# Kernel tuning notes

Measured on AMD Instinct MI355X. Metric: run time of the kernel, lower is better.

## Reference

```python
import jax, jax.numpy as jnp
import numpy as np

H = 128            # hidden_channels
HM = 2 * H         # _inner_mlp_mult * H
N = 50000          # num nodes
E = 400000         # num edges
M = 800000         # num node-edge incidences (2 per edge)
BN_EPS = 1e-5


def _bn_relu(x, g, b):
    # BatchNorm1d in training mode: population stats over the batch dim, then affine + ReLU
    m = x.mean(0)
    v = ((x - m) ** 2).mean(0)
    return jax.nn.relu((x - m) * jax.lax.rsqrt(v + BN_EPS) * g + b)


def setup_inputs() -> dict:
    key = jax.random.key(0)
    ks = jax.random.split(key, 12)
    node_rep = jax.random.normal(ks[0], (N, H), dtype=jnp.float32)
    edge_rep = jax.random.normal(ks[1], (E, H), dtype=jnp.float32)
    src = jax.random.randint(ks[2], (M,), 0, N, dtype=jnp.int32)
    dst = jax.random.randint(ks[3], (M,), 0, E, dtype=jnp.int32)
    node2edge_index = jnp.stack([src, dst], 0)

    def lin(k, fan_in, fan_out):
        return jax.random.normal(k, (fan_in, fan_out), dtype=jnp.float32) / np.sqrt(fan_in)

    return {
        "node_rep": node_rep,
        "edge_rep": edge_rep,
        "node2edge_index": node2edge_index,
        # lvl_mlp_1: Linear(2H->H, no bias), BN(H), ReLU
        "Wa": lin(ks[4], 2 * H, H), "ga": jnp.ones((H,)), "ba": jnp.zeros((H,)),
        # lvl_mlp_2: Linear(H->2H), BN, ReLU, Linear(2H->H), BN, ReLU
        "Wb1": lin(ks[5], H, HM), "gb1": jnp.ones((HM,)), "bb1": jnp.zeros((HM,)),
        "Wb2": lin(ks[6], HM, H), "gb2": jnp.ones((H,)), "bb2": jnp.zeros((H,)),
        # lift_mlp: Linear(H->2H), BN, ReLU, Linear(2H->H), BN, ReLU
        "Wl1": lin(ks[7], H, HM), "gl1": jnp.ones((HM,)), "bl1": jnp.zeros((HM,)),
        "Wl2": lin(ks[8], HM, H), "gl2": jnp.ones((H,)), "bl2": jnp.zeros((H,)),
        "eps1": jnp.zeros(()), "eps2": jnp.zeros(()),
    }


def reference(node_rep, edge_rep, node2edge_index,
              Wa, ga, ba,
              Wb1, gb1, bb1, Wb2, gb2, bb2,
              Wl1, gl1, bl1, Wl2, gl2, bl2,
              eps1, eps2):
    src = node2edge_index[0]  # node index per incidence
    dst = node2edge_index[1]  # edge index per incidence

    # node -> edge gather + scatter_sum
    node2edge_val = node_rep[src]                                   # [M, H]
    lift_aggr = jax.ops.segment_sum(node2edge_val, dst, num_segments=E)  # [E, H]

    # lvl_mlp_1 on concatenated edge features
    lvl_aggr_edge = _bn_relu(jnp.concatenate([lift_aggr, edge_rep], -1) @ Wa, ga, ba)  # [E, H]

    # edge -> node gather + scatter_sum
    lvl_aggr = jax.ops.segment_sum(lvl_aggr_edge[dst], src, num_segments=N)  # [N, H]

    # lvl_mlp_2
    hn = (1.0 + eps1) * node_rep + lvl_aggr
    node_out = _bn_relu(_bn_relu(hn @ Wb1, gb1, bb1) @ Wb2, gb2, bb2)

    # lift_mlp
    he = (1.0 + eps2) * edge_rep + lift_aggr
    edge_out = _bn_relu(_bn_relu(he @ Wl1, gl1, bl1) @ Wl2, gl2, bl2)

    return node_out, edge_out
```

## Files before the change

kernel.cpp:

```cpp
#include <hip/hip_runtime.h>
#include <cstdint>
#include <cstddef>


typedef __bf16 bf16_t;
typedef __bf16 bf16x4 __attribute__((ext_vector_type(4)));
typedef __bf16 bf16x8 __attribute__((ext_vector_type(8)));
typedef float f32x4 __attribute__((ext_vector_type(4)));

__device__ __forceinline__ void atomAddF(float* p, float v) {
  unsafeAtomicAdd(p, v);
}

__device__ __forceinline__ void gload16(const void* g, void* l) {
  __builtin_amdgcn_global_load_lds(
      (const __attribute__((address_space(1))) unsigned int*)g,
      (__attribute__((address_space(3))) unsigned int*)l, 16, 0, 0);
}


__global__ __launch_bounds__(256) void k_hist(
    const int* __restrict__ src, const int* __restrict__ dst, int M,
    int* __restrict__ cnt_e, int* __restrict__ cnt_n) {
  int i = blockIdx.x * blockDim.x + threadIdx.x;
  if (i >= M) return;
  atomicAdd(cnt_e + dst[i], 1);
  atomicAdd(cnt_n + src[i], 1);
}

__global__ __launch_bounds__(256) void k_scan_block(
    const int* __restrict__ in, int* __restrict__ out, int* __restrict__ bsum,
    int L) {
  __shared__ int sh[256];
  int t = threadIdx.x;
  int base = (blockIdx.x * 256 + t) * 4;
  int v[4];
#pragma unroll
  for (int j = 0; j < 4; ++j) v[j] = (base + j < L) ? in[base + j] : 0;
  int tsum = v[0] + v[1] + v[2] + v[3];
  sh[t] = tsum;
  __syncthreads();
#pragma unroll
  for (int off = 1; off < 256; off <<= 1) {
    int x = (t >= off) ? sh[t - off] : 0;
    __syncthreads();
    sh[t] += x;
    __syncthreads();
  }
  int excl = sh[t] - tsum;
  if (t == 255) bsum[blockIdx.x] = sh[255];
  int run = excl;
#pragma unroll
  for (int j = 0; j < 4; ++j) {
    if (base + j < L) out[base + j] = run;
    run += v[j];
  }
}

__global__ __launch_bounds__(1024) void k_scan_top(int* __restrict__ bsum,
                                                   int nb) {
  __shared__ int sh[1024];
  __shared__ int running;
  int t = threadIdx.x;
  if (t == 0) running = 0;
  __syncthreads();
  for (int c = 0; c < nb; c += 1024) {
    int i = c + t;
    int v = (i < nb) ? bsum[i] : 0;
    sh[t] = v;
    __syncthreads();
#pragma unroll
    for (int off = 1; off < 1024; off <<= 1) {
      int x = (t >= off) ? sh[t - off] : 0;
      __syncthreads();
      sh[t] += x;
      __syncthreads();
    }
    int r = running;
    if (i < nb) bsum[i] = r + sh[t] - v;
    __syncthreads();
    if (t == 1023) running = r + sh[1023];
    __syncthreads();
  }
}

__global__ __launch_bounds__(256) void k_scan_add(int* __restrict__ out,
                                                  const int* __restrict__ bsum,
                                                  int L) {
  int base = (blockIdx.x * 256 + threadIdx.x) * 4;
  int add = bsum[blockIdx.x];
#pragma unroll
  for (int j = 0; j < 4; ++j)
    if (base + j < L) out[base + j] += add;
}

__global__ void k_settail(int* off_e, int E, int* off_n, int N, int M) {
  off_e[E] = M;
  off_n[N] = M;
}

__global__ __launch_bounds__(256) void k_fill(
    const int* __restrict__ src, const int* __restrict__ dst, int M,
    const int* __restrict__ off_e, int* __restrict__ fill_e,
    int* __restrict__ csr_e, const int* __restrict__ off_n,
    int* __restrict__ fill_n, int* __restrict__ csr_n) {
  int i = blockIdx.x * blockDim.x + threadIdx.x;
  if (i >= M) return;
  int s = src[i], d = dst[i];
  int pe = off_e[d] + atomicAdd(fill_e + d, 1);
  csr_e[pe] = s;
  int pn = off_n[s] + atomicAdd(fill_n + s, 1);
  csr_n[pn] = d;
}

__global__ __launch_bounds__(256) void k_wconv(const float* __restrict__ W,
                                               bf16_t* __restrict__ Wt, int K,
                                               int NC) {
  int idx = blockIdx.x * blockDim.x + threadIdx.x;
  if (idx >= K * NC) return;
  int k = idx / NC, n = idx % NC;
  Wt[(size_t)n * K + k] = (bf16_t)W[idx];
}

__global__ __launch_bounds__(256) void k_gather1(
    const float* __restrict__ node, const int* __restrict__ off_e,
    const int* __restrict__ csr_e, bf16_t* __restrict__ lift, int E) {
  int e = blockIdx.x * 8 + (threadIdx.x >> 5);
  if (e >= E) return;
  int l = threadIdx.x & 31;
  int b = off_e[e], en = off_e[e + 1];
  float4 acc = make_float4(0.f, 0.f, 0.f, 0.f);
  for (int j = b; j < en; ++j) {
    int r = csr_e[j];
    float4 v = *(const float4*)(node + (size_t)r * 128 + l * 4);
    acc.x += v.x; acc.y += v.y; acc.z += v.z; acc.w += v.w;
  }
  bf16x4 o;
  o[0] = (bf16_t)acc.x; o[1] = (bf16_t)acc.y;
  o[2] = (bf16_t)acc.z; o[3] = (bf16_t)acc.w;
  *(bf16x4*)(lift + (size_t)e * 128 + l * 4) = o;
}

__global__ __launch_bounds__(256) void k_gather2(
    const bf16_t* __restrict__ Y1, const float* __restrict__ st,
    const float* __restrict__ node, const int* __restrict__ off_n,
    const int* __restrict__ csr_n, const float* __restrict__ eps1p,
    bf16_t* __restrict__ hn, int N) {
  int n = blockIdx.x * 16 + (threadIdx.x >> 4);
  if (n >= N) return;
  int l = threadIdx.x & 15;
  float a1 = 1.0f + eps1p[0];
  float4 s0 = *(const float4*)(st + l * 8);
  float4 s1 = *(const float4*)(st + l * 8 + 4);
  float4 t0 = *(const float4*)(st + 128 + l * 8);
  float4 t1 = *(const float4*)(st + 128 + l * 8 + 4);
  float acc[8] = {0.f, 0.f, 0.f, 0.f, 0.f, 0.f, 0.f, 0.f};
  int b = off_n[n], en = off_n[n + 1];
  for (int j = b; j < en; ++j) {
    int r = csr_n[j];
    bf16x8 y = *(const bf16x8*)(Y1 + (size_t)r * 128 + l * 8);
    acc[0] += fmaxf(fmaf((float)y[0], s0.x, t0.x), 0.f);
    acc[1] += fmaxf(fmaf((float)y[1], s0.y, t0.y), 0.f);
    acc[2] += fmaxf(fmaf((float)y[2], s0.z, t0.z), 0.f);
    acc[3] += fmaxf(fmaf((float)y[3], s0.w, t0.w), 0.f);
    acc[4] += fmaxf(fmaf((float)y[4], s1.x, t1.x), 0.f);
    acc[5] += fmaxf(fmaf((float)y[5], s1.y, t1.y), 0.f);
    acc[6] += fmaxf(fmaf((float)y[6], s1.z, t1.z), 0.f);
    acc[7] += fmaxf(fmaf((float)y[7], s1.w, t1.w), 0.f);
  }
  float4 n0 = *(const float4*)(node + (size_t)n * 128 + l * 8);
  float4 n1 = *(const float4*)(node + (size_t)n * 128 + l * 8 + 4);
  bf16x8 hb;
  hb[0] = (bf16_t)fmaf(a1, n0.x, acc[0]);
  hb[1] = (bf16_t)fmaf(a1, n0.y, acc[1]);
  hb[2] = (bf16_t)fmaf(a1, n0.z, acc[2]);
  hb[3] = (bf16_t)fmaf(a1, n0.w, acc[3]);
  hb[4] = (bf16_t)fmaf(a1, n1.x, acc[4]);
  hb[5] = (bf16_t)fmaf(a1, n1.y, acc[5]);
  hb[6] = (bf16_t)fmaf(a1, n1.z, acc[6]);
  hb[7] = (bf16_t)fmaf(a1, n1.w, acc[7]);
  *(bf16x8*)(hn + (size_t)n * 128 + l * 8) = hb;
}


__global__ void k_bnfin(const float* __restrict__ sums, int C, int R,
                        const float* __restrict__ g, const float* __restrict__ b,
                        float* __restrict__ st) {
  int c = blockIdx.x * blockDim.x + threadIdx.x;
  if (c >= C) return;
  float invR = 1.f / (float)R;
  float mean = sums[c] * invR;
  float var = fmaxf(sums[C + c] * invR - mean * mean, 0.f);
  float s = g[c] * rsqrtf(var + 1e-5f);
  st[c] = s;
  st[C + c] = fmaf(-mean, s, b[c]);
}

__global__ __launch_bounds__(256) void k_bnrelu_out(
    const bf16_t* __restrict__ Y, const float* __restrict__ st, long R,
    float* __restrict__ out) {
  long t = (long)blockIdx.x * blockDim.x + threadIdx.x;
  long idx = t * 8;
  if (idx >= R * 128) return;
  int c = (int)(idx & 127);
  bf16x8 y = *(const bf16x8*)(Y + idx);
  float4 s0 = *(const float4*)(st + c);
  float4 s1 = *(const float4*)(st + c + 4);
  float4 t0 = *(const float4*)(st + 128 + c);
  float4 t1 = *(const float4*)(st + 128 + c + 4);
  float4 o0, o1;
  o0.x = fmaxf(fmaf((float)y[0], s0.x, t0.x), 0.f);
  o0.y = fmaxf(fmaf((float)y[1], s0.y, t0.y), 0.f);
  o0.z = fmaxf(fmaf((float)y[2], s0.z, t0.z), 0.f);
  o0.w = fmaxf(fmaf((float)y[3], s0.w, t0.w), 0.f);
  o1.x = fmaxf(fmaf((float)y[4], s1.x, t1.x), 0.f);
  o1.y = fmaxf(fmaf((float)y[5], s1.y, t1.y), 0.f);
  o1.z = fmaxf(fmaf((float)y[6], s1.z, t1.z), 0.f);
  o1.w = fmaxf(fmaf((float)y[7], s1.w, t1.w), 0.f);
  *(float4*)(out + idx) = o0;
  *(float4*)(out + idx + 4) = o1;
}

template <int K, int NC, int TRANSFORM>
__global__ __launch_bounds__(256, 2) void k_gemm_rb(
    const bf16_t* __restrict__ A, const bf16_t* __restrict__ Wt,
    const float* __restrict__ st, float* __restrict__ gstats,
    bf16_t* __restrict__ Y, int R) {
  constexpr int K2 = K * 2;
  constexpr int KF = K / 32;
  constexpr int CTW = NC / 64;
  constexpr int STG = K2 / 64;
  constexpr int TILEB = 64 * K2;
  __shared__ __align__(16) char ldsc[65536];
  const int tid = threadIdx.x;

  for (int p = tid * 16; p < 65536; p += 4096)
    *(float4*)(ldsc + p) = *(const float4*)((const char*)Wt + p);
  __syncthreads();
  const int wv = tid >> 6, lane = tid & 63, quad = lane >> 4, l16 = lane & 15;
  bf16x8 breg[CTW][KF];
#pragma unroll
  for (int ct = 0; ct < CTW; ++ct) {
    const int col = wv * (NC / 4) + ct * 16 + l16;
#pragma unroll
    for (int f = 0; f < KF; ++f)
      breg[ct][f] = *(const bf16x8*)(ldsc + col * K2 + f * 64 + quad * 16);
  }
  __syncthreads();

  int stg_off[STG], stg_row[STG];
#pragma unroll
  for (int j = 0; j < STG; ++j) {
    const int p = j * 1024 + lane * 16;
    const int rl = p / K2;
    const int cg = ((p & (K2 - 1)) >> 4) ^ (rl & 7);
    stg_row[j] = rl;
    stg_off[j] = rl * K2 + cg * 16;
  }
  const int ntiles = (R + 63) >> 6;
  auto stage = [&](int t, int b) {
    char* db = ldsc + b * TILEB + wv * (16 * K2);
    if (t * 64 + 64 <= R) {
      const char* srcb = (const char*)A + (size_t)(t * 64 + wv * 16) * K2;
#pragma unroll
      for (int j = 0; j < STG; ++j) gload16(srcb + stg_off[j], db + j * 1024);
    } else {
#pragma unroll
      for (int j = 0; j < STG; ++j) {
        int g = t * 64 + wv * 16 + stg_row[j];
        if (g > R - 1) g = R - 1;
        gload16((const char*)A + (size_t)g * K2 +
                    (stg_off[j] - stg_row[j] * K2),
                db + j * 1024);
      }
    }
  };

  float csum[CTW], csq[CTW];
#pragma unroll
  for (int ct = 0; ct < CTW; ++ct) { csum[ct] = 0.f; csq[ct] = 0.f; }

  int t = blockIdx.x, b = 0;
  if (t < ntiles) stage(t, 0);
  __syncthreads();
  for (; t < ntiles; t += gridDim.x) {
    const int tn = t + gridDim.x;
    if (tn < ntiles) stage(tn, b ^ 1);
    const char* Ab = ldsc + b * TILEB;
    f32x4 acc[4][CTW] = {};
#pragma unroll
    for (int f = 0; f < KF; ++f) {
      const int csw = ((f * 4 + quad) ^ (l16 & 7)) * 16;
      float4 s0, s1, u0, u1;
      if constexpr (TRANSFORM != 0) {
        const int k = f * 32 + quad * 8;
        s0 = *(const float4*)(st + k);
        s1 = *(const float4*)(st + k + 4);
        u0 = *(const float4*)(st + K + k);
        u1 = *(const float4*)(st + K + k + 4);
      }
#pragma unroll
      for (int rg = 0; rg < 4; ++rg) {
        bf16x8 a = *(const bf16x8*)(Ab + (rg * 16 + l16) * K2 + csw);
        if constexpr (TRANSFORM != 0) {
          bf16x8 o;
          o[0] = (bf16_t)fmaxf(fmaf((float)a[0], s0.x, u0.x), 0.f);
          o[1] = (bf16_t)fmaxf(fmaf((float)a[1], s0.y, u0.y), 0.f);
          o[2] = (bf16_t)fmaxf(fmaf((float)a[2], s0.z, u0.z), 0.f);
          o[3] = (bf16_t)fmaxf(fmaf((float)a[3], s0.w, u0.w), 0.f);
          o[4] = (bf16_t)fmaxf(fmaf((float)a[4], s1.x, u1.x), 0.f);
          o[5] = (bf16_t)fmaxf(fmaf((float)a[5], s1.y, u1.y), 0.f);
          o[6] = (bf16_t)fmaxf(fmaf((float)a[6], s1.z, u1.z), 0.f);
          o[7] = (bf16_t)fmaxf(fmaf((float)a[7], s1.w, u1.w), 0.f);
          a = o;
        }
#pragma unroll
        for (int ct = 0; ct < CTW; ++ct)
          acc[rg][ct] = __builtin_amdgcn_mfma_f32_16x16x32_bf16(
              a, breg[ct][f], acc[rg][ct], 0, 0, 0);
      }
    }
#pragma unroll
    for (int rg = 0; rg < 4; ++rg) {
      const int rowb = t * 64 + rg * 16 + quad * 4;
#pragma unroll
      for (int ct = 0; ct < CTW; ++ct) {
        const int col = wv * (NC / 4) + ct * 16 + l16;
#pragma unroll
        for (int r = 0; r < 4; ++r) {
          const int row = rowb + r;
          if (row < R) {
            const float v = acc[rg][ct][r];
            Y[(size_t)row * NC + col] = (bf16_t)v;
            csum[ct] += v;
            csq[ct] += v * v;
          }
        }
      }
    }
    __syncthreads();
    b ^= 1;
  }
#pragma unroll
  for (int ct = 0; ct < CTW; ++ct) {
    float s = csum[ct], q = csq[ct];
    s += __shfl_xor(s, 16, 64);
    s += __shfl_xor(s, 32, 64);
    q += __shfl_xor(q, 16, 64);
    q += __shfl_xor(q, 32, 64);
    if (quad == 0) {
      const int col = wv * (NC / 4) + ct * 16 + l16;
      atomAddF(gstats + col, s);
      atomAddF(gstats + NC + col, q);
    }
  }
}

__global__ __launch_bounds__(256, 2) void k_gemm_cat_rb(
    const bf16_t* __restrict__ lift, const float* __restrict__ edge,
    const bf16_t* __restrict__ Wt, const float* __restrict__ eps2p,
    float* __restrict__ gstats, bf16_t* __restrict__ Y,
    bf16_t* __restrict__ he, int R) {
  constexpr int KF = 8, CTW = 2;
  __shared__ __align__(16) char ldsc[65536];
  const int tid = threadIdx.x;
  for (int p = tid * 16; p < 65536; p += 4096)
    *(float4*)(ldsc + p) = *(const float4*)((const char*)Wt + p);
  __syncthreads();
  const int wv = tid >> 6, lane = tid & 63, quad = lane >> 4, l16 = lane & 15;
  bf16x8 breg[CTW][KF];
#pragma unroll
  for (int ct = 0; ct < CTW; ++ct) {
    const int col = wv * 32 + ct * 16 + l16;
#pragma unroll
    for (int f = 0; f < KF; ++f)
      breg[ct][f] = *(const bf16x8*)(ldsc + col * 512 + f * 64 + quad * 16);
  }
  __syncthreads();

  const float a2 = 1.0f + eps2p[0];
  const int hi = lane >> 5;
  const int c32 = lane & 31;
  const int ntiles = (R + 63) >> 6;
  float4 ereg[8];
  bf16x4 lreg[8];
  auto loadRegs = [&](int t) {
#pragma unroll
    for (int it = 0; it < 8; ++it) {
      int g = t * 64 + wv * 16 + it * 2 + hi;
      if (g > R - 1) g = R - 1;
      ereg[it] = *(const float4*)(edge + (size_t)g * 128 + c32 * 4);
      lreg[it] = *(const bf16x4*)(lift + (size_t)g * 128 + c32 * 4);
    }
  };
  auto stageHe = [&](int t, int b) {
    char* db = ldsc + b * 32768;
#pragma unroll
    for (int it = 0; it < 8; ++it) {
      const int rl = wv * 16 + it * 2 + hi;
      const int g = t * 64 + rl;
      const float4 e = ereg[it];
      const bf16x4 lv = lreg[it];
      bf16x4 ev, hv;
      ev[0] = (bf16_t)e.x; ev[1] = (bf16_t)e.y;
      ev[2] = (bf16_t)e.z; ev[3] = (bf16_t)e.w;
      hv[0] = (bf16_t)fmaf(a2, e.x, (float)lv[0]);
      hv[1] = (bf16_t)fmaf(a2, e.y, (float)lv[1]);
      hv[2] = (bf16_t)fmaf(a2, e.z, (float)lv[2]);
      hv[3] = (bf16_t)fmaf(a2, e.w, (float)lv[3]);
      if (g < R) *(bf16x4*)(he + (size_t)g * 128 + c32 * 4) = hv;
      const int half = (c32 & 1) * 8;
      const int swl = (((c32 >> 1)) ^ (rl & 7)) * 16 + half;
      const int swe = (((c32 >> 1) + 16) ^ (rl & 7)) * 16 + half;
      *(bf16x4*)(db + rl * 512 + swl) = lv;
      *(bf16x4*)(db + rl * 512 + swe) = ev;
    }
  };

  float csum[CTW] = {0.f, 0.f}, csq[CTW] = {0.f, 0.f};
  int t = blockIdx.x, b = 0;
  if (t < ntiles) {
    loadRegs(t);
    stageHe(t, 0);
  }
  __syncthreads();
  for (; t < ntiles; t += gridDim.x) {
    const int tn = t + gridDim.x;
    if (tn < ntiles) loadRegs(tn);
    const char* Ab = ldsc + b * 32768;
    f32x4 acc[4][CTW] = {};
#pragma unroll
    for (int f = 0; f < KF; ++f) {
      const int csw = ((f * 4 + quad) ^ (l16 & 7)) * 16;
#pragma unroll
      for (int rg = 0; rg < 4; ++rg) {
        bf16x8 a = *(const bf16x8*)(Ab + (rg * 16 + l16) * 512 + csw);
#pragma unroll
        for (int ct = 0; ct < CTW; ++ct)
          acc[rg][ct] = __builtin_amdgcn_mfma_f32_16x16x32_bf16(
              a, breg[ct][f], acc[rg][ct], 0, 0, 0);
      }
    }
#pragma unroll
    for (int rg = 0; rg < 4; ++rg) {
      const int rowb = t * 64 + rg * 16 + quad * 4;
#pragma unroll
      for (int ct = 0; ct < CTW; ++ct) {
        const int col = wv * 32 + ct * 16 + l16;
#pragma unroll
        for (int r = 0; r < 4; ++r) {
          const int row = rowb + r;
          if (row < R) {
            const float v = acc[rg][ct][r];
            Y[(size_t)row * 128 + col] = (bf16_t)v;
            csum[ct] += v;
            csq[ct] += v * v;
          }
        }
      }
    }
    if (tn < ntiles) stageHe(tn, b ^ 1);
    __syncthreads();
    b ^= 1;
  }
#pragma unroll
  for (int ct = 0; ct < CTW; ++ct) {
    float s = csum[ct], q = csq[ct];
    s += __shfl_xor(s, 16, 64);
    s += __shfl_xor(s, 32, 64);
    q += __shfl_xor(q, 16, 64);
    q += __shfl_xor(q, 32, 64);
    if (quad == 0) {
      const int col = wv * 32 + ct * 16 + l16;
      atomAddF(gstats + col, s);
      atomAddF(gstats + 128 + col, q);
    }
  }
}


extern "C" void kernel_launch(void* const* d_in, const int* in_sizes, int n_in,
                              void* d_out, int out_size, void* d_ws,
                              size_t ws_size, hipStream_t stream) {
  const float* node_rep = (const float*)d_in[0];
  const float* edge_rep = (const float*)d_in[1];
  const int* n2e = (const int*)d_in[2];
  const float* Wa = (const float*)d_in[3];
  const float* ga = (const float*)d_in[4];
  const float* ba = (const float*)d_in[5];
  const float* Wb1 = (const float*)d_in[6];
  const float* gb1 = (const float*)d_in[7];
  const float* bb1 = (const float*)d_in[8];
  const float* Wb2 = (const float*)d_in[9];
  const float* gb2 = (const float*)d_in[10];
  const float* bb2 = (const float*)d_in[11];
  const float* Wl1 = (const float*)d_in[12];
  const float* gl1 = (const float*)d_in[13];
  const float* bl1 = (const float*)d_in[14];
  const float* Wl2 = (const float*)d_in[15];
  const float* gl2 = (const float*)d_in[16];
  const float* bl2 = (const float*)d_in[17];
  const float* eps1 = (const float*)d_in[18];
  const float* eps2 = (const float*)d_in[19];

  const int N = in_sizes[0] / 128;
  const int E = in_sizes[1] / 128;
  const int M = in_sizes[2] / 2;
  const int* srcI = n2e;
  const int* dstI = n2e + M;

  char* wsb = (char*)d_ws;
  size_t off = 0;
  auto alloc = [&](size_t bytes) {
    void* p = wsb + off;
    off += (bytes + 255) & ~(size_t)255;
    return p;
  };
  bf16_t* lift = (bf16_t*)alloc((size_t)E * 128 * 2);
  bf16_t* he   = (bf16_t*)alloc((size_t)E * 128 * 2);
  bf16_t* Y1   = (bf16_t*)alloc((size_t)E * 128 * 2);
  bf16_t* Ze   = (bf16_t*)alloc((size_t)E * 256 * 2);
  bf16_t* Y2e  = (bf16_t*)alloc((size_t)E * 128 * 2);
  bf16_t* hn   = (bf16_t*)alloc((size_t)N * 128 * 2);
  bf16_t* Zn   = (bf16_t*)alloc((size_t)N * 256 * 2);
  bf16_t* Y2n  = (bf16_t*)alloc((size_t)N * 128 * 2);
  bf16_t* Wa_t  = (bf16_t*)alloc(256 * 128 * 2);
  bf16_t* Wb1_t = (bf16_t*)alloc(128 * 256 * 2);
  bf16_t* Wb2_t = (bf16_t*)alloc(256 * 128 * 2);
  bf16_t* Wl1_t = (bf16_t*)alloc(128 * 256 * 2);
  bf16_t* Wl2_t = (bf16_t*)alloc(256 * 128 * 2);
  int* zbase  = (int*)alloc(((size_t)E * 2 + (size_t)N * 2 + 8192) * 4);
  int* cnt_e  = zbase;
  int* fill_e = zbase + E;
  int* cnt_n  = zbase + 2 * (size_t)E;
  int* fill_n = zbase + 2 * (size_t)E + N;
  float* stats = (float*)(zbase + 2 * (size_t)E + 2 * (size_t)N);
  int* off_e  = (int*)alloc((size_t)(E + 1) * 4);
  int* csr_e  = (int*)alloc((size_t)M * 4);
  int* off_n  = (int*)alloc((size_t)(N + 1) * 4);
  int* csr_n  = (int*)alloc((size_t)M * 4);
  int* bsumE  = (int*)alloc(4096 * 4);
  int* bsumN  = (int*)alloc(4096 * 4);

  float* sum_a  = stats + 0;
  float* st_a   = stats + 256;
  float* sum_b1 = stats + 512;
  float* st_b1  = stats + 1024;
  float* sum_b2 = stats + 1536;
  float* st_b2  = stats + 1792;
  float* sum_l1 = stats + 2048;
  float* st_l1  = stats + 2560;
  float* sum_l2 = stats + 3072;
  float* st_l2  = stats + 3328;

  float* node_out = (float*)d_out;
  float* edge_out = (float*)d_out + (size_t)N * 128;

  hipMemsetAsync(zbase, 0, ((size_t)E * 2 + (size_t)N * 2 + 8192) * 4, stream);

  k_hist<<<(M + 255) / 256, 256, 0, stream>>>(srcI, dstI, M, cnt_e, cnt_n);
  const int nbE = (E + 1023) / 1024;
  const int nbN = (N + 1023) / 1024;
  k_scan_block<<<nbE, 256, 0, stream>>>(cnt_e, off_e, bsumE, E);
  k_scan_top<<<1, 1024, 0, stream>>>(bsumE, nbE);
  k_scan_add<<<nbE, 256, 0, stream>>>(off_e, bsumE, E);
  k_scan_block<<<nbN, 256, 0, stream>>>(cnt_n, off_n, bsumN, N);
  k_scan_top<<<1, 1024, 0, stream>>>(bsumN, nbN);
  k_scan_add<<<nbN, 256, 0, stream>>>(off_n, bsumN, N);
  k_settail<<<1, 1, 0, stream>>>(off_e, E, off_n, N, M);
  k_fill<<<(M + 255) / 256, 256, 0, stream>>>(srcI, dstI, M, off_e, fill_e,
                                              csr_e, off_n, fill_n, csr_n);

  k_wconv<<<128, 256, 0, stream>>>(Wa, Wa_t, 256, 128);
  k_wconv<<<128, 256, 0, stream>>>(Wb1, Wb1_t, 128, 256);
  k_wconv<<<128, 256, 0, stream>>>(Wb2, Wb2_t, 256, 128);
  k_wconv<<<128, 256, 0, stream>>>(Wl1, Wl1_t, 128, 256);
  k_wconv<<<128, 256, 0, stream>>>(Wl2, Wl2_t, 256, 128);

  const int ntE = (E + 63) / 64, gE = ntE < 512 ? ntE : 512;
  const int ntN = (N + 63) / 64, gN = ntN < 512 ? ntN : 512;

  k_gather1<<<(E + 7) / 8, 256, 0, stream>>>(node_rep, off_e, csr_e, lift, E);

  k_gemm_cat_rb<<<gE, 256, 0, stream>>>(lift, edge_rep, Wa_t, eps2, sum_a, Y1,
                                        he, E);
  k_bnfin<<<1, 256, 0, stream>>>(sum_a, 128, E, ga, ba, st_a);

  k_gather2<<<(N + 15) / 16, 256, 0, stream>>>(Y1, st_a, node_rep, off_n,
                                               csr_n, eps1, hn, N);

  k_gemm_rb<128, 256, 0><<<gN, 256, 0, stream>>>(hn, Wb1_t, nullptr, sum_b1,
                                                 Zn, N);
  k_bnfin<<<1, 256, 0, stream>>>(sum_b1, 256, N, gb1, bb1, st_b1);
  k_gemm_rb<256, 128, 1><<<gN, 256, 0, stream>>>(Zn, Wb2_t, st_b1, sum_b2,
                                                 Y2n, N);
  k_bnfin<<<1, 256, 0, stream>>>(sum_b2, 128, N, gb2, bb2, st_b2);
  {
    long total = ((long)N * 128 + 7) / 8;
    k_bnrelu_out<<<(int)((total + 255) / 256), 256, 0, stream>>>(Y2n, st_b2, N,
                                                                 node_out);
  }

  k_gemm_rb<128, 256, 0><<<gE, 256, 0, stream>>>(he, Wl1_t, nullptr, sum_l1,
                                                 Ze, E);
  k_bnfin<<<1, 256, 0, stream>>>(sum_l1, 256, E, gl1, bl1, st_l1);
  k_gemm_rb<256, 128, 1><<<gE, 256, 0, stream>>>(Ze, Wl2_t, st_l1, sum_l2,
                                                 Y2e, E);
  k_bnfin<<<1, 256, 0, stream>>>(sum_l2, 128, E, gl2, bl2, st_l2);
  {
    long total = ((long)E * 128 + 7) / 8;
    k_bnrelu_out<<<(int)((total + 255) / 256), 256, 0, stream>>>(Y2e, st_l2, E,
                                                                 edge_out);
  }
}
```

Measured before the change: 1.131 ms.

## Triple-buffer GEMM tiles with 32-row tiles, vmcnt waits and vectorized stores

Restructures the row-blocked GEMM into 32-row tiles with a three-buffer staging ring. Fine-grained s_waitcnt vmcnt waits plus raw barriers keep the next tiles' loads in flight while the current tile computes. Weights are loaded into registers in multiple passes through the smaller LDS, which lets occupancy rise to 3 blocks per CU, and the BN scale/shift vectors are cached in LDS. MFMA operands are swapped so each lane holds 4 consecutive columns, enabling packed bf16x4 stores and vector stat accumulation in both GEMM kernels. The risks are more weight-load passes per block and hand-tuned vmcnt counts that must match the exact number of outstanding loads.

After: 1.320 ms. +16.7%, slower.

```diff
diff --git a/kernel.cpp b/kernel.cpp
--- a/kernel.cpp
+++ b/kernel.cpp
@@ -16,6 +16,29 @@
   __builtin_amdgcn_global_load_lds(
       (const __attribute__((address_space(1))) unsigned int*)g,
       (__attribute__((address_space(3))) unsigned int*)l, 16, 0, 0);
+}
+
+template <int N>
+__device__ __forceinline__ void waitVm();
+template <>
+__device__ __forceinline__ void waitVm<0>() {
+  asm volatile("s_waitcnt vmcnt(0)" ::: "memory");
+}
+template <>
+__device__ __forceinline__ void waitVm<8>() {
+  asm volatile("s_waitcnt vmcnt(8)" ::: "memory");
+}
+template <>
+__device__ __forceinline__ void waitVm<12>() {
+  asm volatile("s_waitcnt vmcnt(12)" ::: "memory");
+}
+template <>
+__device__ __forceinline__ void waitVm<16>() {
+  asm volatile("s_waitcnt vmcnt(16)" ::: "memory");
+}
+template <>
+__device__ __forceinline__ void waitVm<18>() {
+  asm volatile("s_waitcnt vmcnt(18)" ::: "memory");
 }
 
 
@@ -222,31 +245,52 @@
 }
 
 template <int K, int NC, int TRANSFORM>
-__global__ __launch_bounds__(256, 2) void k_gemm_rb(
+__global__ __launch_bounds__(256, 3) void k_gemm_rb(
     const bf16_t* __restrict__ A, const bf16_t* __restrict__ Wt,
     const float* __restrict__ st, float* __restrict__ gstats,
     bf16_t* __restrict__ Y, int R) {
   constexpr int K2 = K * 2;
   constexpr int KF = K / 32;
   constexpr int CTW = NC / 64;
-  constexpr int STG = K2 / 64;
-  constexpr int TILEB = 64 * K2;
-  __shared__ __align__(16) char ldsc[65536];
+  constexpr int TR = 32;
+  constexpr int RG = TR / 16;
+  constexpr int TILEB = TR * K2;
+  constexpr int WROWS = TR / 4;
+  constexpr int STG = WROWS * K2 / 1024;
+  constexpr int ST = RG * CTW;
+  constexpr int BTOT = NC * K2;
+  constexpr int REG = 3 * TILEB;
+  constexpr int NPASS = (BTOT + REG - 1) / REG;
+  __shared__ __align__(16) char ldsc[3 * TILEB + K * 8];
   const int tid = threadIdx.x;
-
-  for (int p = tid * 16; p < 65536; p += 4096)
-    *(float4*)(ldsc + p) = *(const float4*)((const char*)Wt + p);
-  __syncthreads();
   const int wv = tid >> 6, lane = tid & 63, quad = lane >> 4, l16 = lane & 15;
+
+  if constexpr (TRANSFORM != 0) {
+    for (int q = tid; q < 2 * K; q += 256)
+      ((float*)(ldsc + 3 * TILEB))[q] = st[q];
+  }
+
   bf16x8 breg[CTW][KF];
-#pragma unroll
-  for (int ct = 0; ct < CTW; ++ct) {
-    const int col = wv * (NC / 4) + ct * 16 + l16;
-#pragma unroll
-    for (int f = 0; f < KF; ++f)
-      breg[ct][f] = *(const bf16x8*)(ldsc + col * K2 + f * 64 + quad * 16);
-  }
-  __syncthreads();
+  const char* Wtb = (const char*)Wt;
+#pragma unroll
+  for (int p = 0; p < NPASS; ++p) {
+    const int base = p * REG;
+    const int lim = (base + REG < BTOT) ? base + REG : BTOT;
+    for (int q = base + tid * 16; q < lim; q += 4096)
+      *(float4*)(ldsc + (q - base)) = *(const float4*)(Wtb + q);
+    __syncthreads();
+#pragma unroll
+    for (int ct = 0; ct < CTW; ++ct) {
+#pragma unroll
+      for (int f = 0; f < KF; ++f) {
+        const int bo =
+            (wv * (NC / 4) + ct * 16 + l16) * K2 + f * 64 + quad * 16;
+        if (bo >= base && bo < lim)
+          breg[ct][f] = *(const bf16x8*)(ldsc + (bo - base));
+      }
+    }
+    __syncthreads();
+  }
 
   int stg_off[STG], stg_row[STG];
 #pragma unroll
@@ -257,17 +301,18 @@
     stg_row[j] = rl;
     stg_off[j] = rl * K2 + cg * 16;
   }
-  const int ntiles = (R + 63) >> 6;
+  const int ntiles = (R + TR - 1) / TR;
+  const int G = gridDim.x;
   auto stage = [&](int t, int b) {
-    char* db = ldsc + b * TILEB + wv * (16 * K2);
-    if (t * 64 + 64 <= R) {
-      const char* srcb = (const char*)A + (size_t)(t * 64 + wv * 16) * K2;
+    char* db = ldsc + b * TILEB + wv * (WROWS * K2);
+    if (t * TR + TR <= R) {
+      const char* srcb = (const char*)A + (size_t)(t * TR + wv * WROWS) * K2;
 #pragma unroll
       for (int j = 0; j < STG; ++j) gload16(srcb + stg_off[j], db + j * 1024);
     } else {
 #pragma unroll
       for (int j = 0; j < STG; ++j) {
-        int g = t * 64 + wv * 16 + stg_row[j];
+        int g = t * TR + wv * WROWS + stg_row[j];
         if (g > R - 1) g = R - 1;
         gload16((const char*)A + (size_t)g * K2 +
                     (stg_off[j] - stg_row[j] * K2),
@@ -276,31 +321,35 @@
     }
   };
 
-  float csum[CTW], csq[CTW];
-#pragma unroll
-  for (int ct = 0; ct < CTW; ++ct) { csum[ct] = 0.f; csq[ct] = 0.f; }
-
-  int t = blockIdx.x, b = 0;
+  f32x4 csum4[CTW] = {}, csq4[CTW] = {};
+  const float* sB = (const float*)(ldsc + 3 * TILEB);
+
+  int t = blockIdx.x;
   if (t < ntiles) stage(t, 0);
-  __syncthreads();
-  for (; t < ntiles; t += gridDim.x) {
-    const int tn = t + gridDim.x;
-    if (tn < ntiles) stage(tn, b ^ 1);
-    const char* Ab = ldsc + b * TILEB;
-    f32x4 acc[4][CTW] = {};
+  if (t + G < ntiles) stage(t + G, 1);
+  waitVm<0>();
+  __builtin_amdgcn_s_barrier();
+  int c = 0;
+  for (; t < ntiles; t += G) {
+    const int t2 = t + 2 * G;
+    const int b2 = (c >= 1) ? c - 1 : c + 2;
+    if (t2 < ntiles) stage(t2, b2);
+
+    const char* Ab = ldsc + c * TILEB;
+    f32x4 acc[RG][CTW] = {};
 #pragma unroll
     for (int f = 0; f < KF; ++f) {
       const int csw = ((f * 4 + quad) ^ (l16 & 7)) * 16;
       float4 s0, s1, u0, u1;
       if constexpr (TRANSFORM != 0) {
         const int k = f * 32 + quad * 8;
-        s0 = *(const float4*)(st + k);
-        s1 = *(const float4*)(st + k + 4);
-        u0 = *(const float4*)(st + K + k);
-        u1 = *(const float4*)(st + K + k + 4);
-      }
-#pragma unroll
-      for (int rg = 0; rg < 4; ++rg) {
+        s0 = *(const float4*)(sB + k);
+        s1 = *(const float4*)(sB + k + 4);
+        u0 = *(const float4*)(sB + K + k);
+        u1 = *(const float4*)(sB + K + k + 4);
+      }
+#pragma unroll
+      for (int rg = 0; rg < RG; ++rg) {
         bf16x8 a = *(const bf16x8*)(Ab + (rg * 16 + l16) * K2 + csw);
         if constexpr (TRANSFORM != 0) {
           bf16x8 o;
@@ -317,41 +366,51 @@
 #pragma unroll
         for (int ct = 0; ct < CTW; ++ct)
           acc[rg][ct] = __builtin_amdgcn_mfma_f32_16x16x32_bf16(
-              a, breg[ct][f], acc[rg][ct], 0, 0, 0);
-      }
-    }
-#pragma unroll
-    for (int rg = 0; rg < 4; ++rg) {
-      const int rowb = t * 64 + rg * 16 + quad * 4;
-#pragma unroll
-      for (int ct = 0; ct < CTW; ++ct) {
-        const int col = wv * (NC / 4) + ct * 16 + l16;
-#pragma unroll
-        for (int r = 0; r < 4; ++r) {
-          const int row = rowb + r;
-          if (row < R) {
-            const float v = acc[rg][ct][r];
-            Y[(size_t)row * NC + col] = (bf16_t)v;
-            csum[ct] += v;
-            csq[ct] += v * v;
-          }
+              breg[ct][f], a, acc[rg][ct], 0, 0, 0);
+      }
+    }
+#pragma unroll
+    for (int rg = 0; rg < RG; ++rg) {
+      const int row = t * TR + rg * 16 + l16;
+      if (row < R) {
+#pragma unroll
+        for (int ct = 0; ct < CTW; ++ct) {
+          const f32x4 v = acc[rg][ct];
+          bf16x4 pv;
+          pv[0] = (bf16_t)v[0]; pv[1] = (bf16_t)v[1];
+          pv[2] = (bf16_t)v[2]; pv[3] = (bf16_t)v[3];
+          *(bf16x4*)(Y + (size_t)row * NC + wv * (NC / 4) + ct * 16 +
+                     quad * 4) = pv;
+          csum4[ct] += v;
+          csq4[ct] += v * v;
         }
       }
     }
-    __syncthreads();
-    b ^= 1;
+    if (t2 < ntiles)
+      waitVm<2 * ST + STG>();
+    else
+      waitVm<2 * ST>();
+    __builtin_amdgcn_s_barrier();
+    c = (c < 2) ? c + 1 : 0;
   }
 #pragma unroll
   for (int ct = 0; ct < CTW; ++ct) {
-    float s = csum[ct], q = csq[ct];
-    s += __shfl_xor(s, 16, 64);
-    s += __shfl_xor(s, 32, 64);
-    q += __shfl_xor(q, 16, 64);
-    q += __shfl_xor(q, 32, 64);
-    if (quad == 0) {
-      const int col = wv * (NC / 4) + ct * 16 + l16;
-      atomAddF(gstats + col, s);
-      atomAddF(gstats + NC + col, q);
+    f32x4 s = csum4[ct], q = csq4[ct];
+#pragma unroll
+    for (int w = 1; w < 16; w <<= 1) {
+#pragma unroll
+      for (int r = 0; r < 4; ++r) {
+        s[r] += __shfl_xor(s[r], w, 64);
+        q[r] += __shfl_xor(q[r], w, 64);
+      }
+    }
+    if (l16 == 0) {
+      const int colb = wv * (NC / 4) + ct * 16 + quad * 4;
+#pragma unroll
+      for (int r = 0; r < 4; ++r) {
+        atomAddF(gstats + colb + r, s[r]);
+        atomAddF(gstats + NC + colb + r, q[r]);
+      }
     }
   }
 }
@@ -417,7 +476,7 @@
     }
   };
 
-  float csum[CTW] = {0.f, 0.f}, csq[CTW] = {0.f, 0.f};
+  f32x4 csum4[CTW] = {}, csq4[CTW] = {};
   int t = blockIdx.x, b = 0;
   if (t < ntiles) {
     loadRegs(t);
@@ -438,24 +497,23 @@
 #pragma unroll
         for (int ct = 0; ct < CTW; ++ct)
           acc[rg][ct] = __builtin_amdgcn_mfma_f32_16x16x32_bf16(
-              a, breg[ct][f], acc[rg][ct], 0, 0, 0);
+              breg[ct][f], a, acc[rg][ct], 0, 0, 0);
       }
     }
 #pragma unroll
     for (int rg = 0; rg < 4; ++rg) {
-      const int rowb = t * 64 + rg * 16 + quad * 4;
-#pragma unroll
-      for (int ct = 0; ct < CTW; ++ct) {
-        const int col = wv * 32 + ct * 16 + l16;
-#pragma unroll
-        for (int r = 0; r < 4; ++r) {
-          const int row = rowb + r;
-          if (row < R) {
-            const float v = acc[rg][ct][r];
-            Y[(size_t)row * 128 + col] = (bf16_t)v;
-            csum[ct] += v;
-            csq[ct] += v * v;
-          }
+      const int row = t * 64 + rg * 16 + l16;
+      if (row < R) {
+#pragma unroll
+        for (int ct = 0; ct < CTW; ++ct) {
+          const f32x4 v = acc[rg][ct];
+          bf16x4 pv;
+          pv[0] = (bf16_t)v[0]; pv[1] = (bf16_t)v[1];
+          pv[2] = (bf16_t)v[2]; pv[3] = (bf16_t)v[3];
+          *(bf16x4*)(Y + (size_t)row * 128 + wv * 32 + ct * 16 + quad * 4) =
+              pv;
+          csum4[ct] += v;
+          csq4[ct] += v * v;
         }
       }
     }
@@ -465,15 +523,22 @@
   }
 #pragma unroll
   for (int ct = 0; ct < CTW; ++ct) {
-    float s = csum[ct], q = csq[ct];
-    s += __shfl_xor(s, 16, 64);
-    s += __shfl_xor(s, 32, 64);
-    q += __shfl_xor(q, 16, 64);
-    q += __shfl_xor(q, 32, 64);
-    if (quad == 0) {
-      const int col = wv * 32 + ct * 16 + l16;
-      atomAddF(gstats + col, s);
-      atomAddF(gstats + 128 + col, q);
+    f32x4 s = csum4[ct], q = csq4[ct];
+#pragma unroll
+    for (int w = 1; w < 16; w <<= 1) {
+#pragma unroll
+      for (int r = 0; r < 4; ++r) {
+        s[r] += __shfl_xor(s[r], w, 64);
+        q[r] += __shfl_xor(q[r], w, 64);
+      }
+    }
+    if (l16 == 0) {
+      const int colb = wv * 32 + ct * 16 + quad * 4;
+#pragma unroll
+      for (int r = 0; r < 4; ++r) {
+        atomAddF(gstats + colb + r, s[r]);
+        atomAddF(gstats + 128 + colb + r, q[r]);
+      }
     }
   }
 }
@@ -577,13 +642,14 @@
   k_wconv<<<128, 256, 0, stream>>>(Wl1, Wl1_t, 128, 256);
   k_wconv<<<128, 256, 0, stream>>>(Wl2, Wl2_t, 256, 128);
 
-  const int ntE = (E + 63) / 64, gE = ntE < 512 ? ntE : 512;
-  const int ntN = (N + 63) / 64, gN = ntN < 512 ? ntN : 512;
+  const int ntE = (E + 31) / 32, gE = ntE < 768 ? ntE : 768;
+  const int ntN = (N + 31) / 32, gN = ntN < 768 ? ntN : 768;
+  const int ntEc = (E + 63) / 64, gEc = ntEc < 512 ? ntEc : 512;
 
   k_gather1<<<(E + 7) / 8, 256, 0, stream>>>(node_rep, off_e, csr_e, lift, E);
 
-  k_gemm_cat_rb<<<gE, 256, 0, stream>>>(lift, edge_rep, Wa_t, eps2, sum_a, Y1,
-                                        he, E);
+  k_gemm_cat_rb<<<gEc, 256, 0, stream>>>(lift, edge_rep, Wa_t, eps2, sum_a,
+                                         Y1, he, E);
   k_bnfin<<<1, 256, 0, stream>>>(sum_a, 128, E, ga, ba, st_a);
 
   k_gather2<<<(N + 15) / 16, 256, 0, stream>>>(Y1, st_a, node_rep, off_n,
```
